# Kernel optimization log

Measured on AMD Instinct MI355X. Metric: run time of the kernel, lower is better.

## Reference

```python
import jax, jax.numpy as jnp
import numpy as np

N = 50000
E = 800000
IN = 256
H = 8
D = 32
NEG_SLOPE = 0.2


def setup_inputs() -> dict:
    key = jax.random.key(0)
    ks = jax.random.split(key, 16)
    inp = {
        "h": jax.random.normal(ks[0], (N, IN), jnp.float32),
        "src_a": jax.random.randint(ks[1], (E,), 0, N),
        "dst_a": jax.random.randint(ks[2], (E,), 0, N),
        "src_b": jax.random.randint(ks[3], (E,), 0, N),
        "dst_b": jax.random.randint(ks[4], (E,), 0, N),
        "W_a": jax.random.normal(ks[5], (IN, H * D), jnp.float32) * 0.05,
        "attn_l_a": jax.random.normal(ks[6], (H, D), jnp.float32) * 0.1,
        "attn_r_a": jax.random.normal(ks[7], (H, D), jnp.float32) * 0.1,
        "bias_a": jax.random.normal(ks[8], (H * D,), jnp.float32) * 0.1,
        "W_b": jax.random.normal(ks[9], (IN, H * D), jnp.float32) * 0.05,
        "attn_l_b": jax.random.normal(ks[10], (H, D), jnp.float32) * 0.1,
        "attn_r_b": jax.random.normal(ks[11], (H, D), jnp.float32) * 0.1,
        "bias_b": jax.random.normal(ks[12], (H * D,), jnp.float32) * 0.1,
        "sem_W1": jax.random.normal(ks[13], (H * D, 128), jnp.float32) * 0.05,
        "sem_b1": jnp.zeros((128,), jnp.float32),
        "sem_W2": jax.random.normal(ks[14], (128, 1), jnp.float32) * 0.1,
    }
    return inp


def gat_conv(h, src, dst, W, attn_l, attn_r, bias):
    # DGL GATConv: project, per-edge additive attention, segment softmax over dst, scatter-agg, bias, ELU
    feat = (h @ W).reshape(N, H, D)                      # [N,H,D]
    el = (feat * attn_l).sum(-1)                          # [N,H]
    er = (feat * attn_r).sum(-1)                          # [N,H]
    e = el[src] + er[dst]                                 # [E,H]
    e = jnp.where(e > 0, e, NEG_SLOPE * e)                # LeakyReLU(0.2)
    m = jax.ops.segment_max(e, dst, num_segments=N)       # [N,H] (-inf for empty)
    ex = jnp.exp(e - m[dst])                              # [E,H]
    denom = jax.ops.segment_sum(ex, dst, num_segments=N)  # [N,H]
    msg = feat[src] * ex[:, :, None]                      # [E,H,D]
    agg = jax.ops.segment_sum(msg, dst, num_segments=N)   # [N,H,D]
    safe = jnp.where(denom > 0, denom, 1.0)
    rst = agg / safe[:, :, None] + bias.reshape(1, H, D)
    rst = jnp.where(rst > 0, rst, jnp.expm1(rst))         # ELU
    return rst.reshape(N, H * D)


def semantic_attention(z, sem_W1, sem_b1, sem_W2):
    # z: [N, M, H*D]
    w = (jnp.tanh(z @ sem_W1 + sem_b1) @ sem_W2).mean(0)  # [M,1]
    beta = jax.nn.softmax(w, axis=0)                      # [M,1]
    return (beta[None] * z).sum(1)                        # [N, H*D]


def reference(h, src_a, dst_a, src_b, dst_b,
              W_a, attn_l_a, attn_r_a, bias_a,
              W_b, attn_l_b, attn_r_b, bias_b,
              sem_W1, sem_b1, sem_W2):
    z_a = gat_conv(h, src_a, dst_a, W_a, attn_l_a, attn_r_a, bias_a)
    z_b = gat_conv(h, src_b, dst_b, W_b, attn_l_b, attn_r_b, bias_b)
    z = jnp.stack([z_a, z_b], axis=1)                     # [N,2,H*D]
    return semantic_attention(z, sem_W1, sem_b1, sem_W2)
```

## Files before the change

### kernel.cpp

```cpp
#include <hip/hip_runtime.h>
#include <math.h>

typedef __attribute__((ext_vector_type(8))) short bf16x8;
typedef __attribute__((ext_vector_type(4))) float f32x4;
typedef __attribute__((ext_vector_type(4))) unsigned short us4;
typedef __attribute__((ext_vector_type(8))) unsigned short us8;

static constexpr int kN  = 50000;
static constexpr int kE  = 800000;
static constexpr int kNBUK = 98;
static constexpr int kCAP  = 9216;

__device__ __forceinline__ float b2f(unsigned short u) {
  union { unsigned u; float f; } x; x.u = ((unsigned)u) << 16; return x.f;
}
__device__ __forceinline__ unsigned short f2b(float f) {
  union { float f; unsigned u; } x; x.f = f;
  unsigned u = x.u;
  unsigned r = (u + 0x7fffu + ((u >> 16) & 1u)) >> 16;
  return (unsigned short)r;
}

__global__ __launch_bounds__(256)
void k_prep(const float* __restrict__ Wa, const float* __restrict__ Wb,
            const float* __restrict__ W1,
            unsigned short* __restrict__ wta, unsigned short* __restrict__ wtb,
            unsigned short* __restrict__ w1t) {
  int b = blockIdx.x, t = threadIdx.x;
  if (b < 256) {
    int i = b * 256 + t, j = i >> 8, k = i & 255;
    wta[j * 256 + k] = f2b(Wa[k * 256 + j]);
  } else if (b < 512) {
    int i = (b - 256) * 256 + t, j = i >> 8, k = i & 255;
    wtb[j * 256 + k] = f2b(Wb[k * 256 + j]);
  } else {
    int i = (b - 512) * 256 + t, j = i >> 8, k = i & 255;
    w1t[j * 256 + k] = f2b(W1[k * 128 + j]);
  }
}

__global__ __launch_bounds__(512, 6)
void k_gemm(const float* __restrict__ h,
            const unsigned short* __restrict__ wta,
            const unsigned short* __restrict__ wtb,
            const float* __restrict__ ala, const float* __restrict__ ara,
            const float* __restrict__ alb, const float* __restrict__ arb,
            unsigned short* __restrict__ fa, unsigned short* __restrict__ fb,
            float* __restrict__ ela, float* __restrict__ era,
            float* __restrict__ elb, float* __restrict__ erb) {
  __shared__ us8 la[64 * 8];
  __shared__ us8 lbb[256 * 8];
  const int z = blockIdx.y;
  const unsigned short* wt = z ? wtb : wta;
  unsigned short* f = z ? fb : fa;
  const float* al = z ? alb : ala;
  const float* ar = z ? arb : ara;
  float* el = z ? elb : ela;
  float* er = z ? erb : era;
  const int m0 = blockIdx.x * 64;
  const int t = threadIdx.x;
  const int lane = t & 63;
  const int wave = t >> 6;
  const int col = lane & 15;
  const int quad = lane >> 4;
  const int nw = wave * 32;
  f32x4 acc[4][2];
#pragma unroll
  for (int i = 0; i < 4; ++i)
#pragma unroll
    for (int j = 0; j < 2; ++j) acc[i][j] = (f32x4){0.f, 0.f, 0.f, 0.f};

  for (int ks = 0; ks < 4; ++ks) {
    const int k0 = ks * 64;
    __syncthreads();
#pragma unroll
    for (int i = 0; i < 2; ++i) {
      int idx = i * 512 + t;
      int r = idx >> 4, g = (idx >> 1) & 7, half = idx & 1;
      int gr = m0 + r;
      f32x4 v = {0.f, 0.f, 0.f, 0.f};
      if (gr < kN) v = *(const f32x4*)(h + (size_t)gr * 256 + k0 + g * 8 + half * 4);
      us4 o;
      o.x = f2b(v.x); o.y = f2b(v.y); o.z = f2b(v.z); o.w = f2b(v.w);
      *(us4*)((unsigned short*)&la[r * 8 + (g ^ (r & 7))] + half * 4) = o;
    }
#pragma unroll
    for (int i = 0; i < 4; ++i) {
      int idx = i * 512 + t;
      int r = idx >> 3, g = idx & 7;
      lbb[r * 8 + (g ^ (r & 7))] = *(const us8*)(wt + r * 256 + k0 + g * 8);
    }
    __syncthreads();
#pragma unroll
    for (int k32 = 0; k32 < 64; k32 += 32) {
      const int cg = (k32 >> 3) + quad;
      bf16x8 af[4], bf[2];
#pragma unroll
      for (int s = 0; s < 4; ++s) {
        int arow = s * 16 + col;
        af[s] = (bf16x8)la[arow * 8 + (cg ^ (arow & 7))];
      }
#pragma unroll
      for (int j = 0; j < 2; ++j) {
        int brow = nw + j * 16 + col;
        bf[j] = (bf16x8)lbb[brow * 8 + (cg ^ (brow & 7))];
      }
#pragma unroll
      for (int i = 0; i < 4; ++i)
#pragma unroll
        for (int j = 0; j < 2; ++j)
          acc[i][j] = __builtin_amdgcn_mfma_f32_16x16x32_bf16(af[i], bf[j],
                                                              acc[i][j], 0, 0, 0);
    }
  }
#pragma unroll
  for (int i = 0; i < 4; ++i) {
#pragma unroll
    for (int r = 0; r < 4; ++r) {
      int row = m0 + i * 16 + quad * 4 + r;
      if (row < kN) {
#pragma unroll
        for (int j = 0; j < 2; ++j)
          f[(size_t)row * 256 + nw + j * 16 + col] = f2b(acc[i][j][r]);
      }
    }
  }
  float alv[2], arv[2];
#pragma unroll
  for (int j = 0; j < 2; ++j) {
    alv[j] = al[nw + j * 16 + col];
    arv[j] = ar[nw + j * 16 + col];
  }
#pragma unroll
  for (int i = 0; i < 4; ++i) {
#pragma unroll
    for (int r = 0; r < 4; ++r) {
      float pl = acc[i][0][r] * alv[0] + acc[i][1][r] * alv[1];
      float pr = acc[i][0][r] * arv[0] + acc[i][1][r] * arv[1];
#pragma unroll
      for (int off = 1; off < 16; off <<= 1) {
        pl += __shfl_xor(pl, off);
        pr += __shfl_xor(pr, off);
      }
      int row = m0 + i * 16 + quad * 4 + r;
      if (col == 0 && row < kN) {
        el[row * 8 + wave] = pl;
        er[row * 8 + wave] = pr;
      }
    }
  }
}

__global__ __launch_bounds__(256)
void k_part(const int* __restrict__ sa, const int* __restrict__ da,
            const int* __restrict__ sb, const int* __restrict__ db,
            int* __restrict__ cnt, unsigned* __restrict__ pay) {
  int y = blockIdx.y;
  const int* s = y ? sb : sa;
  const int* d = y ? db : da;
  unsigned* p = pay + (size_t)y * kNBUK * kCAP;
  int* cn = cnt + y * kNBUK;
  __shared__ unsigned stash[6400];
  __shared__ int h[kNBUK];
  int t = threadIdx.x;
  if (t < kNBUK) h[t] = 0;
  __syncthreads();
  int e0 = blockIdx.x * 6400;
#pragma unroll 5
  for (int it = 0; it < 25; ++it) {
    int e = e0 + it * 256 + t;
    int sv = s[e], dv = d[e];
    int b = dv >> 9;
    stash[it * 256 + t] = (unsigned)sv | ((unsigned)(dv & 511) << 16) |
                          ((unsigned)b << 25);
    atomicAdd(&h[b], 1);
  }
  __syncthreads();
  if (t < kNBUK) h[t] = atomicAdd(&cn[t], h[t]);
  __syncthreads();
#pragma unroll 5
  for (int it = 0; it < 25; ++it) {
    unsigned w = stash[it * 256 + t];
    int b = w >> 25;
    int slot = atomicAdd(&h[b], 1);
    p[b * kCAP + slot] = w & 0x1FFFFFFu;
  }
}

__global__ __launch_bounds__(256)
void k_bscan(const int* __restrict__ cnt, int* __restrict__ bbase,
             int* __restrict__ rpa, int* __restrict__ rpb) {
  __shared__ int buf[2][128];
  int t = threadIdx.x;
  int y = t >> 7, i = t & 127;
  int x = (i < kNBUK) ? cnt[y * kNBUK + i] : 0;
  buf[y][i] = x;
  __syncthreads();
  for (int off = 1; off < 128; off <<= 1) {
    int v = (i >= off) ? buf[y][i - off] : 0;
    __syncthreads();
    buf[y][i] += v;
    __syncthreads();
  }
  if (i < kNBUK) bbase[y * kNBUK + i] = buf[y][i] - x;
  if (t == 0) { rpa[kN] = kE; rpb[kN] = kE; }
}

__global__ __launch_bounds__(256)
void k_bucket(const int* __restrict__ cnt, const int* __restrict__ bbase,
              const unsigned* __restrict__ pay,
              int* __restrict__ rpa, int* __restrict__ rpb,
              int* __restrict__ esa, int* __restrict__ esb) {
  int b = blockIdx.x, y = blockIdx.y;
  int* rp = y ? rpb : rpa;
  int* es = y ? esb : esa;
  const unsigned* p = pay + ((size_t)y * kNBUK + b) * kCAP;
  int c = cnt[y * kNBUK + b];
  int base = bbase[y * kNBUK + b];
  __shared__ unsigned pl[kCAP];
  __shared__ int h[512];
  __shared__ int buf[256];
  int t = threadIdx.x;
  h[t] = 0; h[t + 256] = 0;
  __syncthreads();
  for (int i = t; i < c; i += 256) {
    unsigned w = p[i];
    pl[i] = w;
    atomicAdd(&h[(w >> 16) & 511], 1);
  }
  __syncthreads();
  int a = h[2 * t], b1 = h[2 * t + 1];
  int s2 = a + b1;
  buf[t] = s2;
  __syncthreads();
  for (int off = 1; off < 256; off <<= 1) {
    int v = (t >= off) ? buf[t - off] : 0;
    __syncthreads();
    buf[t] += v;
    __syncthreads();
  }
  int ex = buf[t] - s2;
  int g0 = b * 512 + 2 * t;
  if (g0 < kN) rp[g0] = base + ex;
  if (g0 + 1 < kN) rp[g0 + 1] = base + ex + a;
  h[2 * t] = ex;
  h[2 * t + 1] = ex + a;
  __syncthreads();
  for (int i = t; i < c; i += 256) {
    unsigned w = pl[i];
    int slot = atomicAdd(&h[(w >> 16) & 511], 1);
    es[base + slot] = (int)(w & 0xFFFFu);
  }
}

__global__ __launch_bounds__(256)
void k_agg(const int* __restrict__ rp, const int* __restrict__ es,
           const float* __restrict__ el, const float* __restrict__ er,
           const unsigned short* __restrict__ feat,
           const float* __restrict__ bias,
           float* __restrict__ za, unsigned short* __restrict__ zb,
           int y) {
  __shared__ float wls[4][512];
  __shared__ int sls[4][64];
  int nb = blockIdx.x;
  int lane = threadIdx.x & 63;
  int wave = threadIdx.x >> 6;
  int n = nb * 4 + wave;
  int hh = lane >> 3;
  int h = lane & 7;
  int half = lane >> 5;
  int l5 = lane & 31;
  int h2 = l5 >> 2;
  unsigned idx16 = (unsigned)l5 * 16u;
  float erh = er[n * 8 + h];
  int e0 = rp[n], e1 = rp[n + 1];
  float dsum = 0.f;
  float a0 = 0.f, a1 = 0.f, a2 = 0.f, a3 = 0.f;
  float a4 = 0.f, a5 = 0.f, a6 = 0.f, a7 = 0.f;

  for (int cb = e0; cb < e1; cb += 64) {
    int cnt = e1 - cb;
    if (cnt > 64) cnt = 64;
    for (int it = 0; it * 8 < cnt; ++it) {
      int j = it * 8 + hh;
      if (j < cnt) {
        int s = es[cb + j];
        float ev = *(const float*)((const char*)el + ((unsigned)s << 5) +
                                   ((unsigned)h << 2)) + erh;
        ev = fmaxf(ev, 0.2f * ev);
        float w = __expf(ev);
        wls[wave][it * 64 + lane] = w;
        if (h == 0) sls[wave][j] = s;
        dsum += w;
      }
    }
    int j = 0;
    for (; j + 7 < cnt; j += 8) {
#pragma unroll
      for (int p = 0; p < 4; ++p) {
        int jj = j + 2 * p + half;
        int s = sls[wave][jj];
        float w = wls[wave][jj * 8 + h2];
        us8 fv = *(const us8*)((const char*)feat + (((unsigned)s << 9) + idx16));
        a0 += w * b2f(fv[0]);
        a1 += w * b2f(fv[1]);
        a2 += w * b2f(fv[2]);
        a3 += w * b2f(fv[3]);
        a4 += w * b2f(fv[4]);
        a5 += w * b2f(fv[5]);
        a6 += w * b2f(fv[6]);
        a7 += w * b2f(fv[7]);
      }
    }
    if (j < cnt) {
#pragma unroll
      for (int p = 0; p < 4; ++p) {
        int jj = j + 2 * p + half;
        bool v = jj < cnt;
        int jc = v ? jj : j;
        int s = sls[wave][jc];
        float w = v ? wls[wave][jc * 8 + h2] : 0.f;
        us8 fv = *(const us8*)((const char*)feat + (((unsigned)s << 9) + idx16));
        a0 += w * b2f(fv[0]);
        a1 += w * b2f(fv[1]);
        a2 += w * b2f(fv[2]);
        a3 += w * b2f(fv[3]);
        a4 += w * b2f(fv[4]);
        a5 += w * b2f(fv[5]);
        a6 += w * b2f(fv[6]);
        a7 += w * b2f(fv[7]);
      }
    }
  }
  a0 += __shfl_xor(a0, 32); a1 += __shfl_xor(a1, 32);
  a2 += __shfl_xor(a2, 32); a3 += __shfl_xor(a3, 32);
  a4 += __shfl_xor(a4, 32); a5 += __shfl_xor(a5, 32);
  a6 += __shfl_xor(a6, 32); a7 += __shfl_xor(a7, 32);
  dsum += __shfl_xor(dsum, 8);
  dsum += __shfl_xor(dsum, 16);
  dsum += __shfl_xor(dsum, 32);
  float dh = __shfl(dsum, h2);
  float inv = __builtin_amdgcn_rcpf(dh > 0.f ? dh : 1.f);
  f32x4 blo = *(const f32x4*)(bias + l5 * 8);
  f32x4 bhi = *(const f32x4*)(bias + l5 * 8 + 4);
  float r0 = a0 * inv + blo.x;
  float r1 = a1 * inv + blo.y;
  float r2 = a2 * inv + blo.z;
  float r3 = a3 * inv + blo.w;
  float r4 = a4 * inv + bhi.x;
  float r5 = a5 * inv + bhi.y;
  float r6 = a6 * inv + bhi.z;
  float r7 = a7 * inv + bhi.w;
  r0 = r0 > 0.f ? r0 : __expf(r0) - 1.f;
  r1 = r1 > 0.f ? r1 : __expf(r1) - 1.f;
  r2 = r2 > 0.f ? r2 : __expf(r2) - 1.f;
  r3 = r3 > 0.f ? r3 : __expf(r3) - 1.f;
  r4 = r4 > 0.f ? r4 : __expf(r4) - 1.f;
  r5 = r5 > 0.f ? r5 : __expf(r5) - 1.f;
  r6 = r6 > 0.f ? r6 : __expf(r6) - 1.f;
  r7 = r7 > 0.f ? r7 : __expf(r7) - 1.f;
  f32x4 lo = {r0, r1, r2, r3};
  f32x4 hi = {r4, r5, r6, r7};
  f32x4 ov = half ? hi : lo;
  if (y == 0) {
    *(f32x4*)((char*)za + (size_t)n * 1024 + l5 * 32 + half * 16) = ov;
  } else {
    us4 o;
    o.x = f2b(ov.x); o.y = f2b(ov.y); o.z = f2b(ov.z); o.w = f2b(ov.w);
    *(us4*)((char*)zb + (size_t)n * 512 + l5 * 16 + half * 8) = o;
  }
}

__global__ __launch_bounds__(256)
void k_sem(const float* __restrict__ za,
           const unsigned short* __restrict__ zb,
           const unsigned short* __restrict__ w1t,
           const float* __restrict__ b1,
           const float* __restrict__ W2,
           float* __restrict__ wacc) {
  __shared__ us8 w1l[4096];
  int t = threadIdx.x;
  for (int i = t; i < 4096; i += 256) {
    int j = i >> 5, c = i & 31;
    w1l[j * 32 + (c ^ (j & 7))] = ((const us8*)w1t)[i];
  }
  __syncthreads();
  int lane = t & 63, wave = t >> 6;
  int col = lane & 15, quad = lane >> 4;
  float b1v[8], w2v[8];
#pragma unroll
  for (int tt = 0; tt < 8; ++tt) {
    b1v[tt] = b1[tt * 16 + col];
    w2v[tt] = W2[tt * 16 + col];
  }
  int gw = blockIdx.x * 4 + wave;
  int nw = gridDim.x * 4;
  float sa = 0.f, sb = 0.f;
  for (int gt = gw; gt < 6250; gt += nw) {
    f32x4 acc[8];
#pragma unroll
    for (int tt = 0; tt < 8; ++tt) acc[tt] = (f32x4){0.f, 0.f, 0.f, 0.f};
#pragma unroll
    for (int ks = 0; ks < 8; ++ks) {
      bf16x8 a;
      if (gt < 3125) {
        const float* ap = za + (size_t)gt * 4096 + col * 256 + ks * 32 + quad * 8;
        f32x4 a0 = *(const f32x4*)ap;
        f32x4 a1 = *(const f32x4*)(ap + 4);
        a[0] = (short)f2b(a0.x); a[1] = (short)f2b(a0.y);
        a[2] = (short)f2b(a0.z); a[3] = (short)f2b(a0.w);
        a[4] = (short)f2b(a1.x); a[5] = (short)f2b(a1.y);
        a[6] = (short)f2b(a1.z); a[7] = (short)f2b(a1.w);
      } else {
        a = *(const bf16x8*)(zb + (size_t)(gt - 3125) * 4096 + col * 256 +
                             ks * 32 + quad * 8);
      }
      int c = ks * 4 + quad;
#pragma unroll
      for (int tt = 0; tt < 8; ++tt) {
        int j = tt * 16 + col;
        bf16x8 b = (bf16x8)w1l[j * 32 + (c ^ (j & 7))];
        acc[tt] = __builtin_amdgcn_mfma_f32_16x16x32_bf16(a, b, acc[tt], 0, 0, 0);
      }
    }
    float tot = 0.f;
#pragma unroll
    for (int tt = 0; tt < 8; ++tt)
#pragma unroll
      for (int r = 0; r < 4; ++r) {
        float x = acc[tt][r] + b1v[tt];
        x = fminf(fmaxf(x, -10.f), 10.f);
        float ex = __expf(2.f * x);
        tot += (ex - 1.f) * __builtin_amdgcn_rcpf(ex + 1.f) * w2v[tt];
      }
#pragma unroll
    for (int off = 1; off < 64; off <<= 1) tot += __shfl_xor(tot, off);
    if (gt < 3125) sa += tot; else sb += tot;
  }
  if (lane == 0) {
    if (sa != 0.f) atomicAdd(&wacc[0], sa);
    if (sb != 0.f) atomicAdd(&wacc[1], sb);
  }
}

__global__ __launch_bounds__(256)
void k_combine(const float* __restrict__ za,
               const unsigned short* __restrict__ zb,
               const float* __restrict__ wacc,
               float* __restrict__ out) {
  int i = blockIdx.x * 256 + threadIdx.x;
  float wa = wacc[0] * (1.f / kN), wb = wacc[1] * (1.f / kN);
  float mx = fmaxf(wa, wb);
  float ea = __expf(wa - mx), eb = __expf(wb - mx);
  float inv = __builtin_amdgcn_rcpf(ea + eb);
  float ba = ea * inv, bb = eb * inv;
  f32x4 x = ((const f32x4*)za)[i];
  us4 yv = ((const us4*)zb)[i];
  f32x4 o;
#pragma unroll
  for (int j = 0; j < 4; ++j)
    o[j] = ba * x[j] + bb * b2f(yv[j]);
  ((f32x4*)out)[i] = o;
}

extern "C" void kernel_launch(void* const* d_in, const int* in_sizes, int n_in,
                              void* d_out, int out_size, void* d_ws, size_t ws_size,
                              hipStream_t stream) {
  const float* hin = (const float*)d_in[0];
  const int* src_a = (const int*)d_in[1];
  const int* dst_a = (const int*)d_in[2];
  const int* src_b = (const int*)d_in[3];
  const int* dst_b = (const int*)d_in[4];
  const float* W_a = (const float*)d_in[5];
  const float* al_a = (const float*)d_in[6];
  const float* ar_a = (const float*)d_in[7];
  const float* bias_a = (const float*)d_in[8];
  const float* W_b = (const float*)d_in[9];
  const float* al_b = (const float*)d_in[10];
  const float* ar_b = (const float*)d_in[11];
  const float* bias_b = (const float*)d_in[12];
  const float* sW1 = (const float*)d_in[13];
  const float* sb1 = (const float*)d_in[14];
  const float* sW2 = (const float*)d_in[15];
  float* out = (float*)d_out;

  char* wsb = (char*)d_ws;
  size_t off = 0;
  auto alloc = [&](size_t bytes) -> char* {
    char* p = wsb + off;
    off = (off + bytes + 511) & ~(size_t)511;
    return p;
  };
  unsigned short* feat_a = (unsigned short*)alloc((size_t)kN * 256 * 2);
  unsigned short* feat_b = (unsigned short*)alloc((size_t)kN * 256 * 2);
  unsigned short* z_b    = (unsigned short*)alloc((size_t)kN * 256 * 2);
  float* el_a = (float*)alloc((size_t)kN * 8 * 4);
  float* er_a = (float*)alloc((size_t)kN * 8 * 4);
  float* el_b = (float*)alloc((size_t)kN * 8 * 4);
  float* er_b = (float*)alloc((size_t)kN * 8 * 4);
  unsigned short* wt_a = (unsigned short*)alloc(65536 * 2);
  unsigned short* wt_b = (unsigned short*)alloc(65536 * 2);
  unsigned short* w1t  = (unsigned short*)alloc(32768 * 2);
  int* rp_a = (int*)alloc((size_t)(kN + 1) * 4);
  int* rp_b = (int*)alloc((size_t)(kN + 1) * 4);
  int* es_a = (int*)alloc((size_t)kE * 4);
  int* es_b = (int*)alloc((size_t)kE * 4);
  unsigned* pay = (unsigned*)alloc((size_t)2 * kNBUK * kCAP * 4);
  int* cnt = (int*)alloc((size_t)2 * kNBUK * 4);
  int* bbase = (int*)alloc((size_t)2 * kNBUK * 4);
  float* wacc = (float*)alloc(2 * 4);

  hipMemsetAsync(cnt, 0, (size_t)2 * kNBUK * 4, stream);
  hipMemsetAsync(wacc, 0, 8, stream);

  k_prep<<<640, 256, 0, stream>>>(W_a, W_b, sW1, wt_a, wt_b, w1t);
  k_part<<<dim3(125, 2), 256, 0, stream>>>(src_a, dst_a, src_b, dst_b, cnt, pay);
  k_bscan<<<1, 256, 0, stream>>>(cnt, bbase, rp_a, rp_b);
  k_bucket<<<dim3(kNBUK, 2), 256, 0, stream>>>(cnt, bbase, pay,
                                               rp_a, rp_b, es_a, es_b);
  k_gemm<<<dim3(782, 2), 512, 0, stream>>>(hin, wt_a, wt_b,
                                           al_a, ar_a, al_b, ar_b,
                                           feat_a, feat_b,
                                           el_a, er_a, el_b, er_b);
  k_agg<<<12500, 256, 0, stream>>>(rp_a, es_a, el_a, er_a, feat_a, bias_a,
                                   out, z_b, 0);
  k_agg<<<12500, 256, 0, stream>>>(rp_b, es_b, el_b, er_b, feat_b, bias_b,
                                   out, z_b, 1);
  k_sem<<<512, 256, 0, stream>>>(out, z_b, w1t, sb1, sW2, wacc);
  k_combine<<<12500, 256, 0, stream>>>(out, z_b, wacc, out);
}
```

Measured before the change: 444.7 us.

## Keep W1 slices in registers and stage activation tiles in LDS in k_sem

The semantic-attention kernel no longer loads the full 64KB W1 matrix into shared memory per block. Each wave now keeps its own two 16-column slices of W1 in registers, and the block cooperatively stages one 16-row activation tile (converted to bf16) into a small swizzled LDS buffer. All four waves then share that tile. The small LDS footprint and launch bounds allow more resident blocks, and the grid grows to 2048. The cost is two block barriers per tile and more registers per thread.

```diff
diff --git a/kernel.cpp b/kernel.cpp
--- a/kernel.cpp
+++ b/kernel.cpp
@@ -371,68 +371,78 @@
   }
 }
 
-__global__ __launch_bounds__(256)
+__global__ __launch_bounds__(256, 4)
 void k_sem(const float* __restrict__ za,
            const unsigned short* __restrict__ zb,
            const unsigned short* __restrict__ w1t,
            const float* __restrict__ b1,
            const float* __restrict__ W2,
            float* __restrict__ wacc) {
-  __shared__ us8 w1l[4096];
+  __shared__ us8 al[512];
   int t = threadIdx.x;
-  for (int i = t; i < 4096; i += 256) {
-    int j = i >> 5, c = i & 31;
-    w1l[j * 32 + (c ^ (j & 7))] = ((const us8*)w1t)[i];
-  }
-  __syncthreads();
   int lane = t & 63, wave = t >> 6;
   int col = lane & 15, quad = lane >> 4;
-  float b1v[8], w2v[8];
-#pragma unroll
-  for (int tt = 0; tt < 8; ++tt) {
-    b1v[tt] = b1[tt * 16 + col];
-    w2v[tt] = W2[tt * 16 + col];
-  }
-  int gw = blockIdx.x * 4 + wave;
-  int nw = gridDim.x * 4;
+  bf16x8 breg[2][8];
+  float b1v[2], w2v[2];
+#pragma unroll
+  for (int tl = 0; tl < 2; ++tl) {
+    int j = (wave * 2 + tl) * 16 + col;
+    b1v[tl] = b1[j];
+    w2v[tl] = W2[j];
+#pragma unroll
+    for (int ks = 0; ks < 8; ++ks)
+      breg[tl][ks] = *(const bf16x8*)(w1t + j * 256 + (ks * 4 + quad) * 8);
+  }
   float sa = 0.f, sb = 0.f;
-  for (int gt = gw; gt < 6250; gt += nw) {
-    f32x4 acc[8];
-#pragma unroll
-    for (int tt = 0; tt < 8; ++tt) acc[tt] = (f32x4){0.f, 0.f, 0.f, 0.f};
+  for (int gt = blockIdx.x; gt < 6250; gt += gridDim.x) {
+    __syncthreads();
+    if (gt < 3125) {
+      const float* src = za + (size_t)gt * 4096;
+#pragma unroll
+      for (int i = 0; i < 2; ++i) {
+        int idx = i * 256 + t;
+        int r = idx >> 5, c = idx & 31;
+        f32x4 v0 = *(const f32x4*)(src + r * 256 + c * 8);
+        f32x4 v1 = *(const f32x4*)(src + r * 256 + c * 8 + 4);
+        us8 o;
+        o[0] = (unsigned short)f2b(v0.x); o[1] = (unsigned short)f2b(v0.y);
+        o[2] = (unsigned short)f2b(v0.z); o[3] = (unsigned short)f2b(v0.w);
+        o[4] = (unsigned short)f2b(v1.x); o[5] = (unsigned short)f2b(v1.y);
+        o[6] = (unsigned short)f2b(v1.z); o[7] = (unsigned short)f2b(v1.w);
+        al[r * 32 + (c & 24) + ((c & 7) ^ (r & 7))] = o;
+      }
+    } else {
+      const unsigned short* src = zb + (size_t)(gt - 3125) * 4096;
+#pragma unroll
+      for (int i = 0; i < 2; ++i) {
+        int idx = i * 256 + t;
+        int r = idx >> 5, c = idx & 31;
+        al[r * 32 + (c & 24) + ((c & 7) ^ (r & 7))] =
+            *(const us8*)(src + r * 256 + c * 8);
+      }
+    }
+    __syncthreads();
+    f32x4 acc0 = {0.f, 0.f, 0.f, 0.f};
+    f32x4 acc1 = {0.f, 0.f, 0.f, 0.f};
 #pragma unroll
     for (int ks = 0; ks < 8; ++ks) {
-      bf16x8 a;
-      if (gt < 3125) {
-        const float* ap = za + (size_t)gt * 4096 + col * 256 + ks * 32 + quad * 8;
-        f32x4 a0 = *(const f32x4*)ap;
-        f32x4 a1 = *(const f32x4*)(ap + 4);
-        a[0] = (short)f2b(a0.x); a[1] = (short)f2b(a0.y);
-        a[2] = (short)f2b(a0.z); a[3] = (short)f2b(a0.w);
-        a[4] = (short)f2b(a1.x); a[5] = (short)f2b(a1.y);
-        a[6] = (short)f2b(a1.z); a[7] = (short)f2b(a1.w);
-      } else {
-        a = *(const bf16x8*)(zb + (size_t)(gt - 3125) * 4096 + col * 256 +
-                             ks * 32 + quad * 8);
-      }
       int c = ks * 4 + quad;
-#pragma unroll
-      for (int tt = 0; tt < 8; ++tt) {
-        int j = tt * 16 + col;
-        bf16x8 b = (bf16x8)w1l[j * 32 + (c ^ (j & 7))];
-        acc[tt] = __builtin_amdgcn_mfma_f32_16x16x32_bf16(a, b, acc[tt], 0, 0, 0);
-      }
+      bf16x8 a = (bf16x8)al[col * 32 + (c & 24) + ((c & 7) ^ (col & 7))];
+      acc0 = __builtin_amdgcn_mfma_f32_16x16x32_bf16(a, breg[0][ks], acc0, 0, 0, 0);
+      acc1 = __builtin_amdgcn_mfma_f32_16x16x32_bf16(a, breg[1][ks], acc1, 0, 0, 0);
     }
     float tot = 0.f;
 #pragma unroll
-    for (int tt = 0; tt < 8; ++tt)
-#pragma unroll
-      for (int r = 0; r < 4; ++r) {
-        float x = acc[tt][r] + b1v[tt];
-        x = fminf(fmaxf(x, -10.f), 10.f);
-        float ex = __expf(2.f * x);
-        tot += (ex - 1.f) * __builtin_amdgcn_rcpf(ex + 1.f) * w2v[tt];
-      }
+    for (int r = 0; r < 4; ++r) {
+      float x0 = acc0[r] + b1v[0];
+      x0 = fminf(fmaxf(x0, -10.f), 10.f);
+      float e0 = __expf(2.f * x0);
+      tot += (e0 - 1.f) * __builtin_amdgcn_rcpf(e0 + 1.f) * w2v[0];
+      float x1 = acc1[r] + b1v[1];
+      x1 = fminf(fmaxf(x1, -10.f), 10.f);
+      float e1 = __expf(2.f * x1);
+      tot += (e1 - 1.f) * __builtin_amdgcn_rcpf(e1 + 1.f) * w2v[1];
+    }
 #pragma unroll
     for (int off = 1; off < 64; off <<= 1) tot += __shfl_xor(tot, off);
     if (gt < 3125) sa += tot; else sb += tot;
@@ -526,6 +536,6 @@
                                    out, z_b, 0);
   k_agg<<<12500, 256, 0, stream>>>(rp_b, es_b, el_b, er_b, feat_b, bias_b,
                                    out, z_b, 1);
-  k_sem<<<512, 256, 0, stream>>>(out, z_b, w1t, sb1, sW2, wacc);
+  k_sem<<<2048, 256, 0, stream>>>(out, z_b, w1t, sb1, sW2, wacc);
   k_combine<<<12500, 256, 0, stream>>>(out, z_b, wacc, out);
 }
```

Result: slower. 589.3 us (+32.5%).
